# Kernel optimization log

Hardware: AMD Instinct MI355X
Metric: run time of the kernel (lower is better)

The kernel has to match this reference:

```python
import jax, jax.numpy as jnp
import numpy as np

N = 20000      # nodes
E = 640000     # edges
H = 128        # hidden_channels
F = 128        # num_filters
G = 50         # num_gaussians
L = 6          # num_interactions
CUT = 10.0     # cutoff
NG = 64        # num graphs in batch
NODE_CLASS = 100


def ssp(x):
    # ShiftedSoftplus: softplus(x) - log(2)
    return jax.nn.softplus(x) - jnp.asarray(np.log(2.0), x.dtype)


def setup_inputs() -> dict:
    key = jax.random.key(0)
    ks = jax.random.split(key, 20)
    z = jax.random.randint(ks[0], (N,), 0, NODE_CLASS)
    pos = jax.random.normal(ks[1], (N, 3), dtype=jnp.float32) * 3.0
    edge_index = jax.random.randint(ks[2], (2, E), 0, N)
    batch = jnp.sort(jax.random.randint(ks[3], (N,), 0, NG))
    s = 0.05
    emb = jax.random.normal(ks[4], (NODE_CLASS, H), dtype=jnp.float32) * s
    mlp_w1 = jax.random.normal(ks[5], (L, G, F), dtype=jnp.float32) * s
    mlp_b1 = jnp.zeros((L, F), jnp.float32)
    mlp_w2 = jax.random.normal(ks[6], (L, F, F), dtype=jnp.float32) * s
    mlp_b2 = jnp.zeros((L, F), jnp.float32)
    conv_w1 = jax.random.normal(ks[7], (L, H, F), dtype=jnp.float32) * s
    conv_w2 = jax.random.normal(ks[8], (L, F, H), dtype=jnp.float32) * s
    conv_b2 = jnp.zeros((L, H), jnp.float32)
    lin_w = jax.random.normal(ks[9], (L, H, H), dtype=jnp.float32) * s
    lin_b = jnp.zeros((L, H), jnp.float32)
    out1_w = jax.random.normal(ks[10], (H, H), dtype=jnp.float32) * s
    out1_b = jnp.zeros((H,), jnp.float32)
    out2_w = jax.random.normal(ks[11], (H, H), dtype=jnp.float32) * s
    out2_b = jnp.zeros((H,), jnp.float32)
    return dict(z=z, pos=pos, edge_index=edge_index, batch=batch, emb=emb,
                mlp_w1=mlp_w1, mlp_b1=mlp_b1, mlp_w2=mlp_w2, mlp_b2=mlp_b2,
                conv_w1=conv_w1, conv_w2=conv_w2, conv_b2=conv_b2,
                lin_w=lin_w, lin_b=lin_b,
                out1_w=out1_w, out1_b=out1_b, out2_w=out2_w, out2_b=out2_b)


def reference(z, pos, edge_index, batch, emb,
              mlp_w1, mlp_b1, mlp_w2, mlp_b2,
              conv_w1, conv_w2, conv_b2, lin_w, lin_b,
              out1_w, out1_b, out2_w, out2_b):
    src, dst = edge_index[0], edge_index[1]  # x_j = x[src], aggregate at dst
    h = emb[z]                               # [N, H]
    d = jnp.linalg.norm(pos[src] - pos[dst], axis=-1)  # [E]
    # GaussianSmearing(0, cutoff, G)
    offset = jnp.linspace(0.0, CUT, G).astype(d.dtype)
    coeff = -0.5 / (offset[1] - offset[0]) ** 2
    edge_attr = jnp.exp(coeff * (d[:, None] - offset[None, :]) ** 2)  # [E, G]
    # cosine cutoff
    C = 0.5 * (jnp.cos(d * jnp.pi / CUT) + 1.0)  # [E]
    n = h.shape[0]
    for l in range(L):
        # edge filter: mlp(edge_attr) * C
        W = ssp(edge_attr @ mlp_w1[l] + mlp_b1[l]) @ mlp_w2[l] + mlp_b2[l]
        W = W * C[:, None]                      # [E, F]
        xf = h @ conv_w1[l]                     # lin1, no bias: [N, F]
        msg = xf[src] * W                       # gather + weight
        agg = jax.ops.segment_sum(msg, dst, num_segments=n)  # scatter-add
        x = agg @ conv_w2[l] + conv_b2[l]       # lin2
        x = ssp(x)
        x = x @ lin_w[l] + lin_b[l]
        h = h + x                               # residual
    h = ssp(h @ out1_w + out1_b) @ out2_w + out2_b
    # readout = 'mean'
    sums = jax.ops.segment_sum(h, batch, num_segments=NG)
    cnt = jax.ops.segment_sum(jnp.ones((n,), h.dtype), batch, num_segments=NG)
    return sums / jnp.maximum(cnt, 1.0)[:, None]
```

## Files before the change

kernel.cpp:

```cpp
#include <hip/hip_runtime.h>
#include <math.h>

#define NN 20000
#define NE 640000
#define GDIM 50
#define LAYERS 6
#define NGRAPH 64
#define TBL 2048
#define DMAXF 12.8f
#define G2_PAD 136

typedef __attribute__((ext_vector_type(8))) short short8;
typedef __attribute__((ext_vector_type(4))) float floatx4;

__device__ __forceinline__ float sspf(float x) {
    float sp = (x > 30.0f) ? x : log1pf(expf(x));
    return sp - 0.69314718055994530942f;
}

__device__ __forceinline__ unsigned short f2bs(float f) {
    union { float f; unsigned int i; } u; u.f = f;
    unsigned int r = u.i + 0x7fffu + ((u.i >> 16) & 1u);
    return (unsigned short)(r >> 16);
}

__device__ __forceinline__ float bs2f(unsigned int bits16) {
    union { unsigned int i; float f; } u; u.i = bits16 << 16;
    return u.f;
}

__device__ __forceinline__ short8 pack_bf16x8(float4 a, float4 b) {
    short8 o;
    o[0] = (short)f2bs(a.x); o[1] = (short)f2bs(a.y);
    o[2] = (short)f2bs(a.z); o[3] = (short)f2bs(a.w);
    o[4] = (short)f2bs(b.x); o[5] = (short)f2bs(b.y);
    o[6] = (short)f2bs(b.z); o[7] = (short)f2bs(b.w);
    return o;
}

struct WArgs { const float* s[26]; unsigned short* d[26]; };
#define PREP_WBLK 416
__global__ void prep_a(WArgs a, int* __restrict__ deg, float* __restrict__ out,
                       float* __restrict__ A_tab, const int* __restrict__ z,
                       const float* __restrict__ emb, float* __restrict__ h,
                       const int* __restrict__ batch, float* __restrict__ inv_cnt) {
    __shared__ float tile[32][33];
    int b = blockIdx.x;
    if (b < PREP_WBLK) {
        int mz = b >> 4, sub = b & 15;
        int bx = (sub & 3) * 32, by = (sub >> 2) * 32;
        const float* Wm = a.s[mz];
        unsigned short* Wo = a.d[mz];
        int tx = threadIdx.x & 31, ty = threadIdx.x >> 5;
        for (int r = ty; r < 32; r += 8) tile[r][tx] = Wm[(by + r) * 128 + bx + tx];
        __syncthreads();
        for (int r = ty; r < 32; r += 8) Wo[(bx + r) * 128 + by + tx] = f2bs(tile[tx][r]);
        return;
    }
    int idx = (b - PREP_WBLK) * 256 + threadIdx.x;
    if (idx < NN) { deg[idx] = 0; return; }
    idx -= NN;
    if (idx < NGRAPH * 128) { out[idx] = 0.f; return; }
    idx -= NGRAPH * 128;
    if (idx < (TBL + 2) * GDIM) {
        int i = idx / GDIM, g = idx % GDIM;
        float v = 0.0f;
        if (i <= TBL) {
            float d = (float)i * (DMAXF / (float)TBL);
            float step = 10.0f / 49.0f;
            float off = (float)g * step;
            float coeff = -0.5f / (step * step);
            float dd = d - off;
            v = expf(coeff * dd * dd);
        }
        A_tab[idx] = v;
        return;
    }
    idx -= (TBL + 2) * GDIM;
    if (idx < NN * 32) {
        int n = idx >> 5, q = idx & 31;
        ((float4*)h)[n * 32 + q] = ((const float4*)emb)[(size_t)z[n] * 32 + q];
        return;
    }
    idx -= NN * 32;
    if (idx < NGRAPH) {
        int lo = 0, hi = NN;
        while (lo < hi) { int m = (lo + hi) >> 1; if (batch[m] < idx) lo = m + 1; else hi = m; }
        int lo2 = lo, hi2 = NN;
        while (lo2 < hi2) { int m = (lo2 + hi2) >> 1; if (batch[m] < idx + 1) lo2 = m + 1; else hi2 = m; }
        int cnt = lo2 - lo;
        inv_cnt[idx] = 1.0f / (float)(cnt > 0 ? cnt : 1);
    }
}

__global__ void deg_hist(const int* __restrict__ dst, int* __restrict__ deg) {
    int j = blockIdx.x * blockDim.x + threadIdx.x;
    if (j >= NE) return;
    atomicAdd(&deg[dst[j]], 1);
}

__global__ void scan_a(const int* __restrict__ deg, int* __restrict__ row_ptr,
                       int* __restrict__ bsum) {
    __shared__ int sh[256];
    int b = blockIdx.x, t = threadIdx.x;
    int i = b * 256 + t;
    int v = (i < NN) ? deg[i] : 0;
    int x = v;
    sh[t] = x;
    __syncthreads();
    for (int off = 1; off < 256; off <<= 1) {
        int u = (t >= off) ? sh[t - off] : 0;
        __syncthreads();
        x += u;
        sh[t] = x;
        __syncthreads();
    }
    if (i <= NN) row_ptr[i] = x - v;
    if (t == 255) bsum[b] = x;
}

__global__ void scan_b(const int* __restrict__ bsum, int* __restrict__ row_ptr,
                       int* __restrict__ cursor) {
    __shared__ int spref;
    int b = blockIdx.x, t = threadIdx.x;
    if (t < 64) {
        int s = 0;
        if (t < b) s += bsum[t];
        if (t + 64 < b) s += bsum[t + 64];
        for (int off = 32; off; off >>= 1) s += __shfl_down(s, off);
        if (t == 0) spref = s;
    }
    __syncthreads();
    int prefix = spref;
    int i = b * 256 + t;
    if (i < NN) {
        int v = row_ptr[i] + prefix;
        row_ptr[i] = v;
        cursor[i] = v;
    }
    if (b == 0 && t == 0) row_ptr[NN] = NE;
}

__global__ void csr_fill(const float* __restrict__ pos, const int* __restrict__ src,
                         const int* __restrict__ dst, int* __restrict__ cursor,
                         int2* __restrict__ csr) {
    int j = blockIdx.x * blockDim.x + threadIdx.x;
    if (j >= NE) return;
    int s = src[j], tno = dst[j];
    float dx = pos[3*s+0] - pos[3*tno+0];
    float dy = pos[3*s+1] - pos[3*tno+1];
    float dz = pos[3*s+2] - pos[3*tno+2];
    float d = sqrtf(dx*dx + dy*dy + dz*dz);
    float u = d * ((float)TBL / DMAXF);
    u = fminf(u, (float)(TBL + 1));
    int i0 = (int)u; if (i0 > TBL) i0 = TBL;
    float f = u - (float)i0;
    int p = atomicAdd(&cursor[tno], 1);
    csr[p] = make_int2((i0 << 15) | s, __float_as_int(f));
}

template <int K>
__launch_bounds__(256, 2)
__global__ void gemm_t(const float* __restrict__ A, const float* __restrict__ W,
                       const float* __restrict__ bias, float* __restrict__ Y, int M,
                       int act, int aStride, int wStride, int bStride, int yStride) {
    constexpr int KP = (K + 3) & ~3;
    __shared__ __align__(16) float Ws[KP * 128];
    __shared__ __align__(16) float As[32 * KP];
    int l = blockIdx.y;
    A += (size_t)l * aStride;
    W += (size_t)l * wStride;
    if (bias) bias += (size_t)l * bStride;
    Y += (size_t)l * yStride;
    int t = threadIdx.x;
    int row0 = blockIdx.x * 32;
    for (int i = t; i < KP * 128; i += 256) Ws[i] = (i < K * 128) ? W[i] : 0.0f;
    for (int i = t; i < 32 * KP; i += 256) {
        int r = i / KP, k = i % KP;
        float v = 0.f;
        if (k < K && row0 + r < M) v = A[(size_t)(row0 + r) * K + k];
        As[r * KP + k] = v;
    }
    __syncthreads();
    int tx = t & 31, ty = t >> 5;
    int c0 = tx * 4, r0 = ty * 4;
    float acc[4][4] = {{0.f}};
    #pragma unroll 4
    for (int k = 0; k < KP; k += 4) {
        float4 a0 = *(const float4*)&As[(r0 + 0) * KP + k];
        float4 a1 = *(const float4*)&As[(r0 + 1) * KP + k];
        float4 a2 = *(const float4*)&As[(r0 + 2) * KP + k];
        float4 a3 = *(const float4*)&As[(r0 + 3) * KP + k];
        float4 w0 = *(const float4*)&Ws[(k + 0) * 128 + c0];
        float4 w1 = *(const float4*)&Ws[(k + 1) * 128 + c0];
        float4 w2 = *(const float4*)&Ws[(k + 2) * 128 + c0];
        float4 w3 = *(const float4*)&Ws[(k + 3) * 128 + c0];
        float av[4][4] = {{a0.x,a0.y,a0.z,a0.w},{a1.x,a1.y,a1.z,a1.w},
                          {a2.x,a2.y,a2.z,a2.w},{a3.x,a3.y,a3.z,a3.w}};
        float wv[4][4] = {{w0.x,w0.y,w0.z,w0.w},{w1.x,w1.y,w1.z,w1.w},
                          {w2.x,w2.y,w2.z,w2.w},{w3.x,w3.y,w3.z,w3.w}};
        #pragma unroll
        for (int i = 0; i < 4; i++)
            #pragma unroll
            for (int j = 0; j < 4; j++)
                #pragma unroll
                for (int q = 0; q < 4; q++)
                    acc[i][j] += av[i][q] * wv[q][j];
    }
    float b0 = 0.f, b1 = 0.f, b2 = 0.f, b3 = 0.f;
    if (bias) { b0 = bias[c0]; b1 = bias[c0+1]; b2 = bias[c0+2]; b3 = bias[c0+3]; }
    #pragma unroll
    for (int i = 0; i < 4; i++) {
        int r = row0 + r0 + i;
        if (r >= M) break;
        float4 v;
        v.x = acc[i][0] + b0; v.y = acc[i][1] + b1; v.z = acc[i][2] + b2; v.w = acc[i][3] + b3;
        if (act == 1) { v.x = sspf(v.x); v.y = sspf(v.y); v.z = sspf(v.z); v.w = sspf(v.w); }
        *(float4*)&Y[(size_t)r * 128 + c0] = v;
    }
}

__launch_bounds__(256)
__global__ void gemm_cs2(const float* __restrict__ A1, const unsigned short* __restrict__ W1t,
                         const float* __restrict__ bias1, float* __restrict__ Y1, int M1,
                         const float* __restrict__ A2, const unsigned short* __restrict__ W2t,
                         unsigned short* __restrict__ Yb2, int M2) {
    int y = blockIdx.y;
    const float* A; const unsigned short* Wt; const float* bias;
    float* Yf; unsigned short* Yb; int M;
    if (y < LAYERS) {
        M = M1;
        A = A1 + (size_t)y * M1 * 128;
        Wt = W1t + (size_t)y * 16384;
        bias = bias1 + (size_t)y * 128;
        Yf = Y1 + (size_t)y * M1 * 128;
        Yb = nullptr;
    } else {
        M = M2; A = A2; Wt = W2t; bias = nullptr; Yf = nullptr; Yb = Yb2;
    }
    int wv = threadIdx.x >> 6, lane = threadIdx.x & 63;
    int row0 = blockIdx.x * 32;
    if (row0 >= M) return;
    int lm = lane & 15, lk = (lane >> 4) * 8, orow = (lane >> 4) * 4;
    int r0 = row0 + lm;      r0 = (r0 < M) ? r0 : M - 1;
    int r1 = row0 + 16 + lm; r1 = (r1 < M) ? r1 : M - 1;
    const float* Ap0 = A + (size_t)r0 * 128;
    const float* Ap1 = A + (size_t)r1 * 128;
    short8 af0[4], af1[4];
    #pragma unroll
    for (int kq = 0; kq < 4; kq++) {
        af0[kq] = pack_bf16x8(*(const float4*)(Ap0 + kq * 32 + lk),
                              *(const float4*)(Ap0 + kq * 32 + lk + 4));
        af1[kq] = pack_bf16x8(*(const float4*)(Ap1 + kq * 32 + lk),
                              *(const float4*)(Ap1 + kq * 32 + lk + 4));
    }
    floatx4 acc[2][2];
    #pragma unroll
    for (int i = 0; i < 2; i++)
        #pragma unroll
        for (int j = 0; j < 2; j++) acc[i][j] = (floatx4){0, 0, 0, 0};
    const unsigned short* Wp = Wt + (size_t)(wv * 32) * 128;
    #pragma unroll
    for (int kq = 0; kq < 4; kq++) {
        #pragma unroll
        for (int ct = 0; ct < 2; ct++) {
            short8 bf = *(const short8*)(Wp + (size_t)(ct * 16 + lm) * 128 + kq * 32 + lk);
            acc[0][ct] = __builtin_amdgcn_mfma_f32_16x16x32_bf16(af0[kq], bf, acc[0][ct], 0, 0, 0);
            acc[1][ct] = __builtin_amdgcn_mfma_f32_16x16x32_bf16(af1[kq], bf, acc[1][ct], 0, 0, 0);
        }
    }
    #pragma unroll
    for (int tt = 0; tt < 2; tt++) {
        #pragma unroll
        for (int ct = 0; ct < 2; ct++) {
            int c = wv * 32 + ct * 16 + lm;
            float b = bias ? bias[c] : 0.f;
            #pragma unroll
            for (int r = 0; r < 4; r++) {
                int rr = row0 + tt * 16 + orow + r;
                if (rr >= M) continue;
                float v = acc[tt][ct][r] + b;
                if (Yf) Yf[(size_t)rr * 128 + c] = v;
                if (Yb) Yb[(size_t)rr * 128 + c] = f2bs(v);
            }
        }
    }
}

__launch_bounds__(256)
__global__ void gemm3(const unsigned short* __restrict__ aggb,
                      const unsigned short* __restrict__ W2t, const float* __restrict__ b2,
                      const unsigned short* __restrict__ W3t, const float* __restrict__ b3,
                      const float* __restrict__ resid, float* __restrict__ Yf,
                      const unsigned short* __restrict__ W1nt, unsigned short* __restrict__ xfb) {
    __shared__ unsigned short Ls[16 * G2_PAD];
    int wv = threadIdx.x >> 6, lane = threadIdx.x & 63;
    int row0 = blockIdx.x * 16;
    int lm = lane & 15, lk = (lane >> 4) * 8, orow = (lane >> 4) * 4;
    int cw = wv * 32;
    float rpre[2][4];
    #pragma unroll
    for (int ct = 0; ct < 2; ct++)
        #pragma unroll
        for (int r = 0; r < 4; r++)
            rpre[ct][r] = resid[(size_t)(row0 + orow + r) * 128 + cw + ct * 16 + lm];
    {
        const unsigned short* Ap = aggb + (size_t)(row0 + lm) * 128;
        short8 af[4];
        #pragma unroll
        for (int kq = 0; kq < 4; kq++)
            af[kq] = *(const short8*)(Ap + kq * 32 + lk);
        floatx4 acc[2];
        acc[0] = (floatx4){0, 0, 0, 0}; acc[1] = (floatx4){0, 0, 0, 0};
        const unsigned short* Wp = W2t + (size_t)cw * 128;
        #pragma unroll
        for (int kq = 0; kq < 4; kq++) {
            #pragma unroll
            for (int ct = 0; ct < 2; ct++) {
                short8 bf = *(const short8*)(Wp + (size_t)(ct * 16 + lm) * 128 + kq * 32 + lk);
                acc[ct] = __builtin_amdgcn_mfma_f32_16x16x32_bf16(af[kq], bf, acc[ct], 0, 0, 0);
            }
        }
        #pragma unroll
        for (int ct = 0; ct < 2; ct++) {
            int c = cw + ct * 16 + lm;
            float b = b2[c];
            #pragma unroll
            for (int r = 0; r < 4; r++)
                Ls[(orow + r) * G2_PAD + c] = f2bs(sspf(acc[ct][r] + b));
        }
    }
    __syncthreads();
    float vout[2][4];
    {
        short8 a2[4];
        #pragma unroll
        for (int kq = 0; kq < 4; kq++)
            a2[kq] = *(const short8*)&Ls[lm * G2_PAD + kq * 32 + lk];
        floatx4 acc[2];
        acc[0] = (floatx4){0, 0, 0, 0}; acc[1] = (floatx4){0, 0, 0, 0};
        const unsigned short* Wp = W3t + (size_t)cw * 128;
        #pragma unroll
        for (int kq = 0; kq < 4; kq++) {
            #pragma unroll
            for (int ct = 0; ct < 2; ct++) {
                short8 bf = *(const short8*)(Wp + (size_t)(ct * 16 + lm) * 128 + kq * 32 + lk);
                acc[ct] = __builtin_amdgcn_mfma_f32_16x16x32_bf16(a2[kq], bf, acc[ct], 0, 0, 0);
            }
        }
        #pragma unroll
        for (int ct = 0; ct < 2; ct++) {
            int c = cw + ct * 16 + lm;
            float b = b3[c];
            #pragma unroll
            for (int r = 0; r < 4; r++) {
                int rr = row0 + orow + r;
                float v = acc[ct][r] + b + rpre[ct][r];
                Yf[(size_t)rr * 128 + c] = v;
                vout[ct][r] = v;
            }
        }
    }
    if (!W1nt) return;
    __syncthreads();
    #pragma unroll
    for (int ct = 0; ct < 2; ct++) {
        int c = cw + ct * 16 + lm;
        #pragma unroll
        for (int r = 0; r < 4; r++)
            Ls[(orow + r) * G2_PAD + c] = f2bs(vout[ct][r]);
    }
    __syncthreads();
    {
        short8 a3[4];
        #pragma unroll
        for (int kq = 0; kq < 4; kq++)
            a3[kq] = *(const short8*)&Ls[lm * G2_PAD + kq * 32 + lk];
        floatx4 acc[2];
        acc[0] = (floatx4){0, 0, 0, 0}; acc[1] = (floatx4){0, 0, 0, 0};
        const unsigned short* Wp = W1nt + (size_t)cw * 128;
        #pragma unroll
        for (int kq = 0; kq < 4; kq++) {
            #pragma unroll
            for (int ct = 0; ct < 2; ct++) {
                short8 bf = *(const short8*)(Wp + (size_t)(ct * 16 + lm) * 128 + kq * 32 + lk);
                acc[ct] = __builtin_amdgcn_mfma_f32_16x16x32_bf16(a3[kq], bf, acc[ct], 0, 0, 0);
            }
        }
        #pragma unroll
        for (int ct = 0; ct < 2; ct++) {
            int c = cw + ct * 16 + lm;
            #pragma unroll
            for (int r = 0; r < 4; r++)
                xfb[(size_t)(row0 + orow + r) * 128 + c] = f2bs(acc[ct][r]);
        }
    }
}

__launch_bounds__(256)
__global__ void gemm3h(const float* __restrict__ A,
                       const unsigned short* __restrict__ W2t, const float* __restrict__ b2,
                       const unsigned short* __restrict__ W3t, const float* __restrict__ b3,
                       const int* __restrict__ batch, const float* __restrict__ inv_cnt,
                       float* __restrict__ out) {
    __shared__ unsigned short Ls[16 * G2_PAD];
    int wv = threadIdx.x >> 6, lane = threadIdx.x & 63;
    int row0 = blockIdx.x * 16;
    int lm = lane & 15, lk = (lane >> 4) * 8, orow = (lane >> 4) * 4;
    int cw = wv * 32;
    {
        const float* Ap = A + (size_t)(row0 + lm) * 128;
        short8 af[4];
        #pragma unroll
        for (int kq = 0; kq < 4; kq++)
            af[kq] = pack_bf16x8(*(const float4*)(Ap + kq * 32 + lk),
                                 *(const float4*)(Ap + kq * 32 + lk + 4));
        floatx4 acc[2];
        acc[0] = (floatx4){0, 0, 0, 0}; acc[1] = (floatx4){0, 0, 0, 0};
        const unsigned short* Wp = W2t + (size_t)cw * 128;
        #pragma unroll
        for (int kq = 0; kq < 4; kq++) {
            #pragma unroll
            for (int ct = 0; ct < 2; ct++) {
                short8 bf = *(const short8*)(Wp + (size_t)(ct * 16 + lm) * 128 + kq * 32 + lk);
                acc[ct] = __builtin_amdgcn_mfma_f32_16x16x32_bf16(af[kq], bf, acc[ct], 0, 0, 0);
            }
        }
        #pragma unroll
        for (int ct = 0; ct < 2; ct++) {
            int c = cw + ct * 16 + lm;
            float b = b2[c];
            #pragma unroll
            for (int r = 0; r < 4; r++)
                Ls[(orow + r) * G2_PAD + c] = f2bs(sspf(acc[ct][r] + b));
        }
    }
    __syncthreads();
    float vout[2][4];
    {
        short8 a2[4];
        #pragma unroll
        for (int kq = 0; kq < 4; kq++)
            a2[kq] = *(const short8*)&Ls[lm * G2_PAD + kq * 32 + lk];
        floatx4 acc[2];
        acc[0] = (floatx4){0, 0, 0, 0}; acc[1] = (floatx4){0, 0, 0, 0};
        const unsigned short* Wp = W3t + (size_t)cw * 128;
        #pragma unroll
        for (int kq = 0; kq < 4; kq++) {
            #pragma unroll
            for (int ct = 0; ct < 2; ct++) {
                short8 bf = *(const short8*)(Wp + (size_t)(ct * 16 + lm) * 128 + kq * 32 + lk);
                acc[ct] = __builtin_amdgcn_mfma_f32_16x16x32_bf16(a2[kq], bf, acc[ct], 0, 0, 0);
            }
        }
        #pragma unroll
        for (int ct = 0; ct < 2; ct++) {
            int c = cw + ct * 16 + lm;
            float b = b3[c];
            #pragma unroll
            for (int r = 0; r < 4; r++)
                vout[ct][r] = acc[ct][r] + b;
        }
    }
    int g0  = __builtin_amdgcn_readfirstlane(batch[row0]);
    int g15 = __builtin_amdgcn_readfirstlane(batch[row0 + 15]);
    if (g0 == g15) {
        float inv = inv_cnt[g0];
        #pragma unroll
        for (int ct = 0; ct < 2; ct++) {
            float s = vout[ct][0] + vout[ct][1] + vout[ct][2] + vout[ct][3];
            s += __shfl_xor(s, 16);
            s += __shfl_xor(s, 32);
            if (lane < 16)
                atomicAdd(&out[g0 * 128 + cw + ct * 16 + lm], s * inv);
        }
    } else {
        #pragma unroll
        for (int ct = 0; ct < 2; ct++) {
            int c = cw + ct * 16 + lm;
            #pragma unroll
            for (int r = 0; r < 4; r++) {
                int g = batch[row0 + orow + r];
                atomicAdd(&out[g * 128 + c], vout[ct][r] * inv_cnt[g]);
            }
        }
    }
}

__global__ void tquant(const float* __restrict__ T, unsigned int* __restrict__ Tb) {
    int idx = blockIdx.x * blockDim.x + threadIdx.x;
    const int total = LAYERS * (TBL + 1) * 128;
    if (idx >= total) return;
    int c = idx & 127;
    int li = idx >> 7;
    int i = li % (TBL + 1);
    int l = li / (TBL + 1);
    float d0 = (float)i * (DMAXF / (float)TBL);
    float d1 = (float)(i + 1) * (DMAXF / (float)TBL);
    float C0 = 0.5f * (cosf(d0 * 0.31415926535897931f) + 1.0f);
    float C1 = 0.5f * (cosf(d1 * 0.31415926535897931f) + 1.0f);
    const float* row = T + ((size_t)l * (TBL + 2) + i) * 128 + c;
    float w = row[0] * C0;
    float nw = row[128] * C1;
    Tb[idx] = ((unsigned)f2bs(nw - w) << 16) | f2bs(w);
}

__launch_bounds__(256)
__global__ void edge_agg(const int* __restrict__ row_ptr, const int2* __restrict__ csr,
                         const unsigned int* __restrict__ Tb,
                         const unsigned short* __restrict__ xfb,
                         unsigned short* __restrict__ aggb) {
    int wv = __builtin_amdgcn_readfirstlane(threadIdx.x >> 6);
    int lane = threadIdx.x & 63;
    int n = blockIdx.x * 2 + (wv >> 1);
    int c = (wv & 1) * 64 + lane;
    int e0 = row_ptr[n], e1 = row_ptr[n + 1];
    float ax = 0.f;
    int e = e0;
    for (; e + 16 <= e1; e += 16) {
        unsigned int px[16]; float ff[16];
        #pragma unroll
        for (int q = 0; q < 16; q++) {
            int2 ed = csr[e + q];
            px[q] = (unsigned int)__builtin_amdgcn_readfirstlane(ed.x);
            ff[q] = __int_as_float(__builtin_amdgcn_readfirstlane(ed.y));
        }
        unsigned int tw[16]; unsigned short xv[16];
        #pragma unroll
        for (int q = 0; q < 16; q++) {
            tw[q] = Tb[(px[q] >> 15) * 128 + c];
            xv[q] = xfb[(size_t)(px[q] & 0x7fffu) * 128 + c];
        }
        #pragma unroll
        for (int q = 0; q < 16; q++) {
            float w = bs2f(tw[q] & 0xffffu), dw = bs2f(tw[q] >> 16);
            float x = bs2f((unsigned int)xv[q]);
            ax = fmaf(x, fmaf(ff[q], dw, w), ax);
        }
    }
    for (; e + 4 <= e1; e += 4) {
        unsigned int px[4]; float ff[4];
        #pragma unroll
        for (int q = 0; q < 4; q++) {
            int2 ed = csr[e + q];
            px[q] = (unsigned int)__builtin_amdgcn_readfirstlane(ed.x);
            ff[q] = __int_as_float(__builtin_amdgcn_readfirstlane(ed.y));
        }
        unsigned int tw[4]; unsigned short xv[4];
        #pragma unroll
        for (int q = 0; q < 4; q++) {
            tw[q] = Tb[(px[q] >> 15) * 128 + c];
            xv[q] = xfb[(size_t)(px[q] & 0x7fffu) * 128 + c];
        }
        #pragma unroll
        for (int q = 0; q < 4; q++) {
            float w = bs2f(tw[q] & 0xffffu), dw = bs2f(tw[q] >> 16);
            float x = bs2f((unsigned int)xv[q]);
            ax = fmaf(x, fmaf(ff[q], dw, w), ax);
        }
    }
    for (; e < e1; e++) {
        int2 ed = csr[e];
        unsigned int px = (unsigned int)__builtin_amdgcn_readfirstlane(ed.x);
        float f = __int_as_float(__builtin_amdgcn_readfirstlane(ed.y));
        unsigned int tw = Tb[(px >> 15) * 128 + c];
        unsigned short xv = xfb[(size_t)(px & 0x7fffu) * 128 + c];
        float w = bs2f(tw & 0xffffu), dw = bs2f(tw >> 16);
        float x = bs2f((unsigned int)xv);
        ax = fmaf(x, fmaf(f, dw, w), ax);
    }
    aggb[(size_t)n * 128 + c] = f2bs(ax);
}

extern "C" void kernel_launch(void* const* d_in, const int* in_sizes, int n_in,
                              void* d_out, int out_size, void* d_ws, size_t ws_size,
                              hipStream_t stream) {
    const int*   z       = (const int*)d_in[0];
    const float* pos     = (const float*)d_in[1];
    const int*   eidx    = (const int*)d_in[2];
    const int*   src     = eidx;
    const int*   dst     = eidx + NE;
    const int*   batch   = (const int*)d_in[3];
    const float* emb     = (const float*)d_in[4];
    const float* mlp_w1  = (const float*)d_in[5];
    const float* mlp_b1  = (const float*)d_in[6];
    const float* mlp_w2  = (const float*)d_in[7];
    const float* mlp_b2  = (const float*)d_in[8];
    const float* conv_w1 = (const float*)d_in[9];
    const float* conv_w2 = (const float*)d_in[10];
    const float* conv_b2 = (const float*)d_in[11];
    const float* lin_w   = (const float*)d_in[12];
    const float* lin_b   = (const float*)d_in[13];
    const float* out1_w  = (const float*)d_in[14];
    const float* out1_b  = (const float*)d_in[15];
    const float* out2_w  = (const float*)d_in[16];
    const float* out2_b  = (const float*)d_in[17];
    float* out = (float*)d_out;

    char* wp = (char*)d_ws;
    auto alloc = [&](size_t bytes) {
        char* p = wp;
        wp += (bytes + 255) & ~(size_t)255;
        return p;
    };
    const int Mt = TBL + 2;
    int*    deg     = (int*)alloc(NN * 4);
    int*    row_ptr = (int*)alloc((NN + 1) * 4);
    int*    cursor  = (int*)alloc(NN * 4);
    int*    bsum    = (int*)alloc(128 * 4);
    float*  inv_cnt = (float*)alloc(NGRAPH * 4);
    int2*   csr     = (int2*)alloc((size_t)NE * 8);
    float*  A_tab   = (float*)alloc((size_t)Mt * GDIM * 4);
    float*  T1all   = (float*)alloc((size_t)LAYERS * Mt * 128 * 4);
    float*  T       = (float*)alloc((size_t)LAYERS * Mt * 128 * 4);
    unsigned int* Tb = (unsigned int*)alloc((size_t)LAYERS * (TBL + 1) * 128 * 4);
    float*  h       = (float*)alloc((size_t)NN * 128 * 4);
    unsigned short* aggb = (unsigned short*)alloc((size_t)NN * 128 * 2);
    unsigned short* xfb  = (unsigned short*)alloc((size_t)NN * 128 * 2);
    unsigned short* wbf  = (unsigned short*)alloc((size_t)26 * 16384 * 2);
    unsigned short* mlp_w2t  = wbf;
    unsigned short* conv_w1t = wbf + (size_t)6 * 16384;
    unsigned short* conv_w2t = wbf + (size_t)12 * 16384;
    unsigned short* lin_wt   = wbf + (size_t)18 * 16384;
    unsigned short* out1_wt  = wbf + (size_t)24 * 16384;
    unsigned short* out2_wt  = wbf + (size_t)25 * 16384;

    WArgs wa;
    for (int l = 0; l < 6; l++) {
        wa.s[l]      = mlp_w2  + (size_t)l * 16384;  wa.d[l]      = mlp_w2t  + (size_t)l * 16384;
        wa.s[6 + l]  = conv_w1 + (size_t)l * 16384;  wa.d[6 + l]  = conv_w1t + (size_t)l * 16384;
        wa.s[12 + l] = conv_w2 + (size_t)l * 16384;  wa.d[12 + l] = conv_w2t + (size_t)l * 16384;
        wa.s[18 + l] = lin_w   + (size_t)l * 16384;  wa.d[18 + l] = lin_wt   + (size_t)l * 16384;
    }
    wa.s[24] = out1_w; wa.d[24] = out1_wt;
    wa.s[25] = out2_w; wa.d[25] = out2_wt;
    const int initN = NN + NGRAPH * 128 + Mt * GDIM + NN * 32 + NGRAPH;
    prep_a<<<PREP_WBLK + (initN + 255) / 256, 256, 0, stream>>>(wa, deg, out, A_tab, z,
                                                                emb, h, batch, inv_cnt);

    deg_hist<<<(NE + 255) / 256, 256, 0, stream>>>(dst, deg);
    const int NB = (NN + 255) / 256;
    scan_a<<<NB, 256, 0, stream>>>(deg, row_ptr, bsum);
    scan_b<<<NB, 256, 0, stream>>>(bsum, row_ptr, cursor);
    csr_fill<<<(NE + 255) / 256, 256, 0, stream>>>(pos, src, dst, cursor, csr);

    const int gt32 = (Mt + 31) / 32;
    gemm_t<GDIM><<<dim3(gt32, LAYERS), 256, 0, stream>>>(
        A_tab, mlp_w1, mlp_b1, T1all, Mt, 1, 0, GDIM * 128, 128, Mt * 128);
    gemm_cs2<<<dim3(NN / 32, LAYERS + 1), 256, 0, stream>>>(
        T1all, mlp_w2t, mlp_b2, T, Mt,
        h, conv_w1t, xfb, NN);
    tquant<<<(LAYERS * (TBL + 1) * 128 + 255) / 256, 256, 0, stream>>>(T, Tb);

    const int gn = NN / 16;
    for (int l = 0; l < LAYERS; l++) {
        edge_agg<<<NN / 2, 256, 0, stream>>>(row_ptr, csr,
                                             Tb + (size_t)l * (TBL + 1) * 128, xfb, aggb);
        const unsigned short* w1n = (l + 1 < LAYERS) ? conv_w1t + (size_t)(l + 1) * 16384 : nullptr;
        gemm3<<<gn, 256, 0, stream>>>(aggb, conv_w2t + (size_t)l * 16384, conv_b2 + l * 128,
                                      lin_wt + (size_t)l * 16384, lin_b + l * 128,
                                      h, h, w1n, xfb);
    }

    gemm3h<<<gn, 256, 0, stream>>>(h, out1_wt, out1_b, out2_wt, out2_b,
                                   batch, inv_cnt, out);
}
```

Before: 525.9 us.

## Fuse filter-table construction into a single build_tb kernel per layer

Replaces the separate Gaussian table init, first MLP GEMM, second MLP GEMM and tquant kernels with one kernel that computes Gaussian features, both MLP layers, the cosine cutoff and the bf16 delta packing in shared memory per 32-row tile. This removes the intermediate A_tab, T1all and T buffers and two kernel launches. The second MLP layer is now done with scalar FMAs instead of MFMA, and each block recomputes one extra halo row. The node lin1 GEMM is split into its own simpler gemm_cs kernel.

```diff
diff --git a/kernel.cpp b/kernel.cpp
--- a/kernel.cpp
+++ b/kernel.cpp
@@ -41,9 +41,9 @@
 struct WArgs { const float* s[26]; unsigned short* d[26]; };
 #define PREP_WBLK 416
 __global__ void prep_a(WArgs a, int* __restrict__ deg, float* __restrict__ out,
-                       float* __restrict__ A_tab, const int* __restrict__ z,
-                       const float* __restrict__ emb, float* __restrict__ h,
-                       const int* __restrict__ batch, float* __restrict__ inv_cnt) {
+                       const int* __restrict__ z, const float* __restrict__ emb,
+                       float* __restrict__ h, const int* __restrict__ batch,
+                       float* __restrict__ inv_cnt) {
     __shared__ float tile[32][33];
     int b = blockIdx.x;
     if (b < PREP_WBLK) {
@@ -62,21 +62,6 @@
     idx -= NN;
     if (idx < NGRAPH * 128) { out[idx] = 0.f; return; }
     idx -= NGRAPH * 128;
-    if (idx < (TBL + 2) * GDIM) {
-        int i = idx / GDIM, g = idx % GDIM;
-        float v = 0.0f;
-        if (i <= TBL) {
-            float d = (float)i * (DMAXF / (float)TBL);
-            float step = 10.0f / 49.0f;
-            float off = (float)g * step;
-            float coeff = -0.5f / (step * step);
-            float dd = d - off;
-            v = expf(coeff * dd * dd);
-        }
-        A_tab[idx] = v;
-        return;
-    }
-    idx -= (TBL + 2) * GDIM;
     if (idx < NN * 32) {
         int n = idx >> 5, q = idx & 31;
         ((float4*)h)[n * 32 + q] = ((const float4*)emb)[(size_t)z[n] * 32 + q];
@@ -159,93 +144,79 @@
     csr[p] = make_int2((i0 << 15) | s, __float_as_int(f));
 }
 
-template <int K>
-__launch_bounds__(256, 2)
-__global__ void gemm_t(const float* __restrict__ A, const float* __restrict__ W,
-                       const float* __restrict__ bias, float* __restrict__ Y, int M,
-                       int act, int aStride, int wStride, int bStride, int yStride) {
-    constexpr int KP = (K + 3) & ~3;
-    __shared__ __align__(16) float Ws[KP * 128];
-    __shared__ __align__(16) float As[32 * KP];
+__launch_bounds__(256)
+__global__ void build_tb(const float* __restrict__ mlp_w1, const float* __restrict__ mlp_b1,
+                         const unsigned short* __restrict__ mlp_w2t,
+                         const float* __restrict__ mlp_b2, unsigned int* __restrict__ Tb) {
+    __shared__ float W1s[GDIM * 128];
+    __shared__ float gs[33 * 52];
+    __shared__ float t1s[33 * 130];
+    __shared__ float Ts[33 * 130];
     int l = blockIdx.y;
-    A += (size_t)l * aStride;
-    W += (size_t)l * wStride;
-    if (bias) bias += (size_t)l * bStride;
-    Y += (size_t)l * yStride;
+    int row0 = blockIdx.x * 32;
+    const float* w1 = mlp_w1 + (size_t)l * GDIM * 128;
+    const float* b1 = mlp_b1 + (size_t)l * 128;
+    const unsigned short* w2t = mlp_w2t + (size_t)l * 16384;
+    const float* b2 = mlp_b2 + (size_t)l * 128;
+    unsigned int* tb = Tb + (size_t)l * (TBL + 1) * 128;
     int t = threadIdx.x;
-    int row0 = blockIdx.x * 32;
-    for (int i = t; i < KP * 128; i += 256) Ws[i] = (i < K * 128) ? W[i] : 0.0f;
-    for (int i = t; i < 32 * KP; i += 256) {
-        int r = i / KP, k = i % KP;
+    for (int i = t; i < GDIM * 128; i += 256) W1s[i] = w1[i];
+    for (int i = t; i < 33 * GDIM; i += 256) {
+        int r = i / GDIM, g = i % GDIM;
+        int row = row0 + r;
         float v = 0.f;
-        if (k < K && row0 + r < M) v = A[(size_t)(row0 + r) * K + k];
-        As[r * KP + k] = v;
-    }
-    __syncthreads();
-    int tx = t & 31, ty = t >> 5;
-    int c0 = tx * 4, r0 = ty * 4;
-    float acc[4][4] = {{0.f}};
-    #pragma unroll 4
-    for (int k = 0; k < KP; k += 4) {
-        float4 a0 = *(const float4*)&As[(r0 + 0) * KP + k];
-        float4 a1 = *(const float4*)&As[(r0 + 1) * KP + k];
-        float4 a2 = *(const float4*)&As[(r0 + 2) * KP + k];
-        float4 a3 = *(const float4*)&As[(r0 + 3) * KP + k];
-        float4 w0 = *(const float4*)&Ws[(k + 0) * 128 + c0];
-        float4 w1 = *(const float4*)&Ws[(k + 1) * 128 + c0];
-        float4 w2 = *(const float4*)&Ws[(k + 2) * 128 + c0];
-        float4 w3 = *(const float4*)&Ws[(k + 3) * 128 + c0];
-        float av[4][4] = {{a0.x,a0.y,a0.z,a0.w},{a1.x,a1.y,a1.z,a1.w},
-                          {a2.x,a2.y,a2.z,a2.w},{a3.x,a3.y,a3.z,a3.w}};
-        float wv[4][4] = {{w0.x,w0.y,w0.z,w0.w},{w1.x,w1.y,w1.z,w1.w},
-                          {w2.x,w2.y,w2.z,w2.w},{w3.x,w3.y,w3.z,w3.w}};
-        #pragma unroll
-        for (int i = 0; i < 4; i++)
-            #pragma unroll
-            for (int j = 0; j < 4; j++)
-                #pragma unroll
-                for (int q = 0; q < 4; q++)
-                    acc[i][j] += av[i][q] * wv[q][j];
-    }
-    float b0 = 0.f, b1 = 0.f, b2 = 0.f, b3 = 0.f;
-    if (bias) { b0 = bias[c0]; b1 = bias[c0+1]; b2 = bias[c0+2]; b3 = bias[c0+3]; }
-    #pragma unroll
-    for (int i = 0; i < 4; i++) {
-        int r = row0 + r0 + i;
-        if (r >= M) break;
-        float4 v;
-        v.x = acc[i][0] + b0; v.y = acc[i][1] + b1; v.z = acc[i][2] + b2; v.w = acc[i][3] + b3;
-        if (act == 1) { v.x = sspf(v.x); v.y = sspf(v.y); v.z = sspf(v.z); v.w = sspf(v.w); }
-        *(float4*)&Y[(size_t)r * 128 + c0] = v;
+        if (row <= TBL) {
+            float d = (float)row * (DMAXF / (float)TBL);
+            const float step = 10.0f / 49.0f;
+            const float coeff = -0.5f / (step * step);
+            float dd = d - (float)g * step;
+            v = expf(coeff * dd * dd);
+        }
+        gs[r * 52 + g] = v;
+    }
+    __syncthreads();
+    for (int i = t; i < 33 * 128; i += 256) {
+        int r = i >> 7, c = i & 127;
+        float acc = b1[c];
+        #pragma unroll 5
+        for (int g = 0; g < GDIM; g++)
+            acc = fmaf(gs[r * 52 + g], W1s[g * 128 + c], acc);
+        t1s[r * 130 + c] = sspf(acc);
+    }
+    __syncthreads();
+    for (int i = t; i < 33 * 128; i += 256) {
+        int r = i >> 7, c = i & 127;
+        const unsigned short* wr = w2t + (size_t)c * 128;
+        const float* tr = &t1s[r * 130];
+        float acc = b2[c];
+        #pragma unroll 8
+        for (int k = 0; k < 128; k++)
+            acc = fmaf(tr[k], bs2f((unsigned)wr[k]), acc);
+        Ts[r * 130 + c] = acc;
+    }
+    __syncthreads();
+    for (int i = t; i < 32 * 128; i += 256) {
+        int r = i >> 7, c = i & 127;
+        int row = row0 + r;
+        if (row > TBL) continue;
+        float d0 = (float)row * (DMAXF / (float)TBL);
+        float d1 = (float)(row + 1) * (DMAXF / (float)TBL);
+        float C0 = 0.5f * (cosf(d0 * 0.31415926535897931f) + 1.0f);
+        float C1 = 0.5f * (cosf(d1 * 0.31415926535897931f) + 1.0f);
+        float w  = Ts[r * 130 + c] * C0;
+        float nw = Ts[(r + 1) * 130 + c] * C1;
+        tb[(size_t)row * 128 + c] = ((unsigned)f2bs(nw - w) << 16) | f2bs(w);
     }
 }
 
 __launch_bounds__(256)
-__global__ void gemm_cs2(const float* __restrict__ A1, const unsigned short* __restrict__ W1t,
-                         const float* __restrict__ bias1, float* __restrict__ Y1, int M1,
-                         const float* __restrict__ A2, const unsigned short* __restrict__ W2t,
-                         unsigned short* __restrict__ Yb2, int M2) {
-    int y = blockIdx.y;
-    const float* A; const unsigned short* Wt; const float* bias;
-    float* Yf; unsigned short* Yb; int M;
-    if (y < LAYERS) {
-        M = M1;
-        A = A1 + (size_t)y * M1 * 128;
-        Wt = W1t + (size_t)y * 16384;
-        bias = bias1 + (size_t)y * 128;
-        Yf = Y1 + (size_t)y * M1 * 128;
-        Yb = nullptr;
-    } else {
-        M = M2; A = A2; Wt = W2t; bias = nullptr; Yf = nullptr; Yb = Yb2;
-    }
+__global__ void gemm_cs(const float* __restrict__ A, const unsigned short* __restrict__ Wt,
+                        unsigned short* __restrict__ Yb) {
     int wv = threadIdx.x >> 6, lane = threadIdx.x & 63;
     int row0 = blockIdx.x * 32;
-    if (row0 >= M) return;
     int lm = lane & 15, lk = (lane >> 4) * 8, orow = (lane >> 4) * 4;
-    int r0 = row0 + lm;      r0 = (r0 < M) ? r0 : M - 1;
-    int r1 = row0 + 16 + lm; r1 = (r1 < M) ? r1 : M - 1;
-    const float* Ap0 = A + (size_t)r0 * 128;
-    const float* Ap1 = A + (size_t)r1 * 128;
+    const float* Ap0 = A + (size_t)(row0 + lm) * 128;
+    const float* Ap1 = A + (size_t)(row0 + 16 + lm) * 128;
     short8 af0[4], af1[4];
     #pragma unroll
     for (int kq = 0; kq < 4; kq++) {
@@ -274,14 +245,10 @@
         #pragma unroll
         for (int ct = 0; ct < 2; ct++) {
             int c = wv * 32 + ct * 16 + lm;
-            float b = bias ? bias[c] : 0.f;
             #pragma unroll
             for (int r = 0; r < 4; r++) {
                 int rr = row0 + tt * 16 + orow + r;
-                if (rr >= M) continue;
-                float v = acc[tt][ct][r] + b;
-                if (Yf) Yf[(size_t)rr * 128 + c] = v;
-                if (Yb) Yb[(size_t)rr * 128 + c] = f2bs(v);
+                Yb[(size_t)rr * 128 + c] = f2bs(acc[tt][ct][r]);
             }
         }
     }
@@ -485,24 +452,6 @@
             }
         }
     }
-}
-
-__global__ void tquant(const float* __restrict__ T, unsigned int* __restrict__ Tb) {
-    int idx = blockIdx.x * blockDim.x + threadIdx.x;
-    const int total = LAYERS * (TBL + 1) * 128;
-    if (idx >= total) return;
-    int c = idx & 127;
-    int li = idx >> 7;
-    int i = li % (TBL + 1);
-    int l = li / (TBL + 1);
-    float d0 = (float)i * (DMAXF / (float)TBL);
-    float d1 = (float)(i + 1) * (DMAXF / (float)TBL);
-    float C0 = 0.5f * (cosf(d0 * 0.31415926535897931f) + 1.0f);
-    float C1 = 0.5f * (cosf(d1 * 0.31415926535897931f) + 1.0f);
-    const float* row = T + ((size_t)l * (TBL + 2) + i) * 128 + c;
-    float w = row[0] * C0;
-    float nw = row[128] * C1;
-    Tb[idx] = ((unsigned)f2bs(nw - w) << 16) | f2bs(w);
 }
 
 __launch_bounds__(256)
@@ -603,16 +552,12 @@
         wp += (bytes + 255) & ~(size_t)255;
         return p;
     };
-    const int Mt = TBL + 2;
     int*    deg     = (int*)alloc(NN * 4);
     int*    row_ptr = (int*)alloc((NN + 1) * 4);
     int*    cursor  = (int*)alloc(NN * 4);
     int*    bsum    = (int*)alloc(128 * 4);
     float*  inv_cnt = (float*)alloc(NGRAPH * 4);
     int2*   csr     = (int2*)alloc((size_t)NE * 8);
-    float*  A_tab   = (float*)alloc((size_t)Mt * GDIM * 4);
-    float*  T1all   = (float*)alloc((size_t)LAYERS * Mt * 128 * 4);
-    float*  T       = (float*)alloc((size_t)LAYERS * Mt * 128 * 4);
     unsigned int* Tb = (unsigned int*)alloc((size_t)LAYERS * (TBL + 1) * 128 * 4);
     float*  h       = (float*)alloc((size_t)NN * 128 * 4);
     unsigned short* aggb = (unsigned short*)alloc((size_t)NN * 128 * 2);
@@ -634,8 +579,8 @@
     }
     wa.s[24] = out1_w; wa.d[24] = out1_wt;
     wa.s[25] = out2_w; wa.d[25] = out2_wt;
-    const int initN = NN + NGRAPH * 128 + Mt * GDIM + NN * 32 + NGRAPH;
-    prep_a<<<PREP_WBLK + (initN + 255) / 256, 256, 0, stream>>>(wa, deg, out, A_tab, z,
+    const int initN = NN + NGRAPH * 128 + NN * 32 + NGRAPH;
+    prep_a<<<PREP_WBLK + (initN + 255) / 256, 256, 0, stream>>>(wa, deg, out, z,
                                                                 emb, h, batch, inv_cnt);
 
     deg_hist<<<(NE + 255) / 256, 256, 0, stream>>>(dst, deg);
@@ -644,13 +589,9 @@
     scan_b<<<NB, 256, 0, stream>>>(bsum, row_ptr, cursor);
     csr_fill<<<(NE + 255) / 256, 256, 0, stream>>>(pos, src, dst, cursor, csr);
 
-    const int gt32 = (Mt + 31) / 32;
-    gemm_t<GDIM><<<dim3(gt32, LAYERS), 256, 0, stream>>>(
-        A_tab, mlp_w1, mlp_b1, T1all, Mt, 1, 0, GDIM * 128, 128, Mt * 128);
-    gemm_cs2<<<dim3(NN / 32, LAYERS + 1), 256, 0, stream>>>(
-        T1all, mlp_w2t, mlp_b2, T, Mt,
-        h, conv_w1t, xfb, NN);
-    tquant<<<(LAYERS * (TBL + 1) * 128 + 255) / 256, 256, 0, stream>>>(T, Tb);
+    build_tb<<<dim3((TBL + 32) / 32, LAYERS), 256, 0, stream>>>(
+        mlp_w1, mlp_b1, mlp_w2t, mlp_b2, Tb);
+    gemm_cs<<<NN / 32, 256, 0, stream>>>(h, conv_w1t, xfb);
 
     const int gn = NN / 16;
     for (int l = 0; l < LAYERS; l++) {
```

Measured after the change: 581.1 us. +10.5%, slower.
